# Kernel tuning notes

Measured on AMD Instinct MI355X. Metric: run time of the kernel, lower is better.

The kernel has to match this reference:

```python
import jax, jax.numpy as jnp
import numpy as np

# RReLU in eval mode == LeakyReLU with slope (lower+upper)/2, defaults 1/8, 1/3
RRELU_SLOPE = (1.0 / 8.0 + 1.0 / 3.0) / 2.0


def rrelu(x):
    return jnp.where(x >= 0, x, x * RRELU_SLOPE)


def _linear_params(key, fan_in, fan_out):
    kw, kb = jax.random.split(key)
    s = 1.0 / np.sqrt(fan_in)
    W = jax.random.uniform(kw, (fan_in, fan_out), minval=-s, maxval=s, dtype=jnp.float32)
    b = jax.random.uniform(kb, (fan_out,), minval=-s, maxval=s, dtype=jnp.float32)
    return W, b


def setup_inputs() -> dict:
    key = jax.random.key(0)
    ks = jax.random.split(key, 6)
    B, L, D_TS, D_SEQ, HID = 64, 2048, 8, 120, 64
    DIN = D_TS + D_SEQ
    ts = jax.random.normal(ks[0], (B, L, D_TS), dtype=jnp.float32)
    seq = jax.random.normal(ks[1], (B, L, D_SEQ), dtype=jnp.float32)
    lengths = jax.random.randint(ks[2], (B,), 1, L + 1, dtype=jnp.int32)
    Wk, bk = _linear_params(ks[3], DIN, HID)
    Wq, bq = _linear_params(ks[4], DIN, HID)
    Wv, bv = _linear_params(ks[5], DIN, HID)
    return {"ts": ts, "seq": seq, "lengths": lengths,
            "Wk": Wk, "bk": bk, "Wq": Wq, "bq": bq, "Wv": Wv, "bv": bv}


def reference(ts, seq, lengths, Wk, bk, Wq, bq, Wv, bv):
    # packed_cat([ts, seq]) -> concat along feature dim; padded positions masked later
    x = jnp.concatenate([ts, seq], axis=-1)              # [B, L, Din]
    k = rrelu(jnp.einsum('bld,dh->blh', x, Wk) + bk)     # [B, L, H]
    v = rrelu(jnp.einsum('bld,dh->blh', x, Wv) + bv)     # [B, L, H]
    q = rrelu(jnp.einsum('bld,dh->blh', x, Wq) + bq)     # [B, L, H]
    B, L, _ = x.shape
    # get_last_vectors_unpadded: last valid token of each sequence
    q_last = q[jnp.arange(B), lengths - 1]               # [B, H]
    scores = jnp.einsum('bh,blh->bl', q_last, k)         # [B, L]
    valid = jnp.arange(L)[None, :] < lengths[:, None]    # [B, L]
    scores = jnp.where(valid, scores, -jnp.inf)
    attn = jax.nn.softmax(scores, axis=-1)               # masked softmax over seq
    return jnp.einsum('bl,blh->bh', attn, v)             # [B, H]
```

## Files before the change

### kernel.cpp

```cpp
#include <hip/hip_runtime.h>
#include <hip/hip_bf16.h>

#define B_   64
#define L_   2048
#define DTS  8
#define DSEQ 120
#define DIN  128
#define H_   64
#define TILE 64
#define NT   (L_ / TILE)

typedef unsigned short u16;
typedef __bf16 bf16x8 __attribute__((ext_vector_type(8)));
typedef float  f32x4  __attribute__((ext_vector_type(4)));

__device__ __forceinline__ float rrelu_f(float x) {
    return x >= 0.f ? x : x * 0.22916666666666666f;
}

__device__ __forceinline__ u16 f2bf(float x) {
    unsigned u = __float_as_uint(x);
    return (u16)((u + 0x7FFFu + ((u >> 16) & 1u)) >> 16);
}
__device__ __forceinline__ float bf2f(u16 u) {
    return __uint_as_float(((unsigned)u) << 16);
}

__global__ void prep_kernel(const float* __restrict__ Wk, const float* __restrict__ Wv,
                            u16* __restrict__ pkh, u16* __restrict__ pkl,
                            u16* __restrict__ pvh, u16* __restrict__ pvl)
{
    const int f = blockIdx.x * 256 + threadIdx.x;
    const int idx = f & 8191;
    const bool isK = f < 8192;
    const float* W = isK ? Wk : Wv;
    u16* hi = isK ? pkh : pvh;
    u16* lo = isK ? pkl : pvl;
    const int j = idx & 7, lane = (idx >> 3) & 63, kk = (idx >> 9) & 3, ni = idx >> 11;
    const int kd = kk * 32 + (lane >> 4) * 8 + j;
    const int n  = ni * 16 + (lane & 15);
    const float v = W[kd * H_ + n];
    const u16 h = f2bf(v);
    hi[idx] = h;
    lo[idx] = f2bf(v - bf2f(h));
}

__global__ void qlast_kernel(const float* __restrict__ ts, const float* __restrict__ seq,
                             const int* __restrict__ lengths,
                             const float* __restrict__ Wq, const float* __restrict__ bq,
                             float* __restrict__ qlast)
{
    const int b = blockIdx.x, h = threadIdx.x;
    const int l = lengths[b] - 1;
    const float* tsr = ts  + ((size_t)b * L_ + l) * DTS;
    const float* sqr = seq + ((size_t)b * L_ + l) * DSEQ;
    float acc = bq[h];
    #pragma unroll
    for (int d = 0; d < DTS; ++d)  acc += tsr[d] * Wq[d * H_ + h];
    for (int d = 0; d < DSEQ; ++d) acc += sqr[d] * Wq[(DTS + d) * H_ + h];
    qlast[b * H_ + h] = rrelu_f(acc);
}

__global__ __launch_bounds__(256) void tile_kernel(
    const float* __restrict__ ts, const float* __restrict__ seq,
    const int* __restrict__ lengths,
    const u16* __restrict__ pkh, const u16* __restrict__ pkl,
    const u16* __restrict__ pvh, const u16* __restrict__ pvl,
    const float* __restrict__ bk, const float* __restrict__ bv,
    const float* __restrict__ qlast,
    float* __restrict__ pm, float* __restrict__ pd, float* __restrict__ pacc)
{
    const int b = blockIdx.y, t = blockIdx.x;
    const int tid = threadIdx.x;
    const int len = lengths[b];
    const int ls = t * TILE;
    const int pbase = b * NT + t;

    if (ls >= len) {
        if (tid < H_) pacc[(size_t)pbase * H_ + tid] = 0.f;
        if (tid == 0) { pm[pbase] = -INFINITY; pd[pbase] = 0.f; }
        return;
    }
    const int nv = min(TILE, len - ls);

    __shared__ __align__(16) u16 xh[TILE][136];
    __shared__ __align__(16) u16 xl[TILE][136];
    __shared__ float k_s[TILE][65];
    __shared__ float v_s[TILE][65];
    __shared__ float qls[H_];
    __shared__ float sc[TILE];
    __shared__ float red[4][H_];

    for (int c = tid; c < TILE * 32; c += 256) {
        const int row = c >> 5, ch = c & 31;
        const float* src = (ch < 2)
            ? ts  + ((size_t)b * L_ + ls + row) * DTS  + ch * 4
            : seq + ((size_t)b * L_ + ls + row) * DSEQ + (ch - 2) * 4;
        const float4 v = *(const float4*)src;
        const u16 h0 = f2bf(v.x), h1 = f2bf(v.y), h2 = f2bf(v.z), h3 = f2bf(v.w);
        const u16 g0 = f2bf(v.x - bf2f(h0)), g1 = f2bf(v.y - bf2f(h1));
        const u16 g2 = f2bf(v.z - bf2f(h2)), g3 = f2bf(v.w - bf2f(h3));
        unsigned* ph = (unsigned*)&xh[row][ch * 4];
        unsigned* pl = (unsigned*)&xl[row][ch * 4];
        ph[0] = (unsigned)h0 | ((unsigned)h1 << 16);
        ph[1] = (unsigned)h2 | ((unsigned)h3 << 16);
        pl[0] = (unsigned)g0 | ((unsigned)g1 << 16);
        pl[1] = (unsigned)g2 | ((unsigned)g3 << 16);
    }
    if (tid < H_) qls[tid] = qlast[b * H_ + tid];
    __syncthreads();

    const int wave = tid >> 6, lane = tid & 63;
    const int quad = lane >> 4, l16 = lane & 15;
    const int m0 = wave * 16;

    const u16* hrow = &xh[m0 + l16][0];
    const u16* lrow = &xl[m0 + l16][0];
    bf16x8 ah[4], al[4];
    #pragma unroll
    for (int kk = 0; kk < 4; ++kk) {
        ah[kk] = *(const bf16x8*)(hrow + kk * 32 + quad * 8);
        al[kk] = *(const bf16x8*)(lrow + kk * 32 + quad * 8);
    }

    #pragma unroll
    for (int ni = 0; ni < 4; ++ni) {
        const int n = ni * 16 + l16;
        f32x4 ak = {0.f, 0.f, 0.f, 0.f};
        f32x4 av = {0.f, 0.f, 0.f, 0.f};
        #pragma unroll
        for (int kk = 0; kk < 4; ++kk) {
            const size_t off = (size_t)(((ni * 4 + kk) * 64 + lane)) * 8;
            const bf16x8 bkh = *(const bf16x8*)(pkh + off);
            const bf16x8 bkl = *(const bf16x8*)(pkl + off);
            const bf16x8 bvh = *(const bf16x8*)(pvh + off);
            const bf16x8 bvl = *(const bf16x8*)(pvl + off);
            ak = __builtin_amdgcn_mfma_f32_16x16x32_bf16(ah[kk], bkh, ak, 0, 0, 0);
            ak = __builtin_amdgcn_mfma_f32_16x16x32_bf16(al[kk], bkh, ak, 0, 0, 0);
            ak = __builtin_amdgcn_mfma_f32_16x16x32_bf16(ah[kk], bkl, ak, 0, 0, 0);
            av = __builtin_amdgcn_mfma_f32_16x16x32_bf16(ah[kk], bvh, av, 0, 0, 0);
            av = __builtin_amdgcn_mfma_f32_16x16x32_bf16(al[kk], bvh, av, 0, 0, 0);
            av = __builtin_amdgcn_mfma_f32_16x16x32_bf16(ah[kk], bvl, av, 0, 0, 0);
        }
        const float bbk = bk[n], bbv = bv[n];
        #pragma unroll
        for (int r = 0; r < 4; ++r) {
            const int row = m0 + quad * 4 + r;
            k_s[row][n] = rrelu_f(ak[r] + bbk);
            v_s[row][n] = rrelu_f(av[r] + bbv);
        }
    }
    __syncthreads();

    if (wave == 0) {
        const int l = lane;
        float s = 0.f;
        #pragma unroll 8
        for (int h = 0; h < H_; ++h) s += qls[h] * k_s[l][h];
        if (l >= nv) s = -INFINITY;
        float m = s;
        #pragma unroll
        for (int off = 32; off; off >>= 1) m = fmaxf(m, __shfl_xor(m, off));
        const float p = __expf(s - m);
        float d = p;
        #pragma unroll
        for (int off = 32; off; off >>= 1) d += __shfl_xor(d, off);
        sc[l] = p;
        if (lane == 0) { pm[pbase] = m; pd[pbase] = d; }
    }
    __syncthreads();

    {
        const int h = lane;
        float acc = 0.f;
        #pragma unroll
        for (int i = 0; i < 16; ++i)
            acc += sc[wave * 16 + i] * v_s[wave * 16 + i][h];
        red[wave][h] = acc;
    }
    __syncthreads();
    if (tid < H_)
        pacc[(size_t)pbase * H_ + tid] = red[0][tid] + red[1][tid] + red[2][tid] + red[3][tid];
}

__global__ void combine_kernel(const float* __restrict__ pm, const float* __restrict__ pd,
                               const float* __restrict__ pacc, float* __restrict__ out)
{
    const int b = blockIdx.x, h = threadIdx.x;
    float m = -INFINITY;
    for (int t = 0; t < NT; ++t) m = fmaxf(m, pm[b * NT + t]);
    float den = 0.f, num = 0.f;
    for (int t = 0; t < NT; ++t) {
        const float w = __expf(pm[b * NT + t] - m);
        den += pd[b * NT + t] * w;
        num += pacc[(size_t)(b * NT + t) * H_ + h] * w;
    }
    out[b * H_ + h] = num / den;
}

extern "C" void kernel_launch(void* const* d_in, const int* in_sizes, int n_in,
                              void* d_out, int out_size, void* d_ws, size_t ws_size,
                              hipStream_t stream)
{
    const float* ts      = (const float*)d_in[0];
    const float* seq     = (const float*)d_in[1];
    const int*   lengths = (const int*)d_in[2];
    const float* Wk      = (const float*)d_in[3];
    const float* bk      = (const float*)d_in[4];
    const float* Wq      = (const float*)d_in[5];
    const float* bq      = (const float*)d_in[6];
    const float* Wv      = (const float*)d_in[7];
    const float* bv      = (const float*)d_in[8];

    float* ws    = (float*)d_ws;
    float* qlast = ws;
    float* pm    = ws + 4096;
    float* pd    = ws + 6144;
    float* pacc  = ws + 8192;
    u16*  packw  = (u16*)(ws + 139264);
    u16* pkh = packw;
    u16* pkl = packw + 8192;
    u16* pvh = packw + 16384;
    u16* pvl = packw + 24576;

    prep_kernel<<<dim3(64), dim3(256), 0, stream>>>(Wk, Wv, pkh, pkl, pvh, pvl);
    qlast_kernel<<<dim3(B_), dim3(H_), 0, stream>>>(ts, seq, lengths, Wq, bq, qlast);
    tile_kernel<<<dim3(NT, B_), dim3(256), 0, stream>>>(ts, seq, lengths,
                                                        pkh, pkl, pvh, pvl, bk, bv,
                                                        qlast, pm, pd, pacc);
    combine_kernel<<<dim3(B_), dim3(H_), 0, stream>>>(pm, pd, pacc, (float*)d_out);
}
```

Before: 145.3 us.

## Fuse setup kernels, DMA x to LDS, register-resident K/V, last-block combine

Merges the weight-packing and q_last kernels into one setup launch. The combine step is folded into the tile kernel through a per-batch atomic counter, so the last finishing block does the final reduction. Each block now handles two tiles and loads x with global_load_lds into swizzled fp32 LDS, splitting it into bf16 hi/lo in registers. Scores and the P·V product are computed from MFMA accumulators with shuffles instead of staging K and V through shared memory. This removes two launches and much LDS traffic, at the cost of atomics and fewer blocks in the grid.

Result: slower. 251.2 us (+72.8%).

```diff
diff --git a/kernel.cpp b/kernel.cpp
--- a/kernel.cpp
+++ b/kernel.cpp
@@ -5,19 +5,20 @@
 #define L_   2048
 #define DTS  8
 #define DSEQ 120
-#define DIN  128
 #define H_   64
 #define TILE 64
-#define NT   (L_ / TILE)
+#define NT   32
+#define TPB  2
+#define GX   (NT/TPB)
 
 typedef unsigned short u16;
 typedef __bf16 bf16x8 __attribute__((ext_vector_type(8)));
+typedef short  short8 __attribute__((ext_vector_type(8)));
 typedef float  f32x4  __attribute__((ext_vector_type(4)));
 
 __device__ __forceinline__ float rrelu_f(float x) {
     return x >= 0.f ? x : x * 0.22916666666666666f;
 }
-
 __device__ __forceinline__ u16 f2bf(float x) {
     unsigned u = __float_as_uint(x);
     return (u16)((u + 0x7FFFu + ((u >> 16) & 1u)) >> 16);
@@ -25,177 +26,229 @@
 __device__ __forceinline__ float bf2f(u16 u) {
     return __uint_as_float(((unsigned)u) << 16);
 }
-
-__global__ void prep_kernel(const float* __restrict__ Wk, const float* __restrict__ Wv,
-                            u16* __restrict__ pkh, u16* __restrict__ pkl,
-                            u16* __restrict__ pvh, u16* __restrict__ pvl)
+__device__ __forceinline__ void dma16(void* lds, const void* g) {
+    __builtin_amdgcn_global_load_lds(
+        (const __attribute__((address_space(1))) unsigned*)g,
+        (__attribute__((address_space(3))) unsigned*)lds, 16, 0, 0);
+}
+
+__global__ void setup_kernel(const float* __restrict__ ts, const float* __restrict__ seq,
+                             const int* __restrict__ lengths,
+                             const float* __restrict__ Wk, const float* __restrict__ Wv,
+                             const float* __restrict__ Wq, const float* __restrict__ bq,
+                             u16* __restrict__ pkh, u16* __restrict__ pkl,
+                             u16* __restrict__ pvh, u16* __restrict__ pvl,
+                             float* __restrict__ qlast, unsigned* __restrict__ cnt)
 {
-    const int f = blockIdx.x * 256 + threadIdx.x;
-    const int idx = f & 8191;
-    const bool isK = f < 8192;
-    const float* W = isK ? Wk : Wv;
-    u16* hi = isK ? pkh : pvh;
-    u16* lo = isK ? pkl : pvl;
-    const int j = idx & 7, lane = (idx >> 3) & 63, kk = (idx >> 9) & 3, ni = idx >> 11;
-    const int kd = kk * 32 + (lane >> 4) * 8 + j;
-    const int n  = ni * 16 + (lane & 15);
-    const float v = W[kd * H_ + n];
-    const u16 h = f2bf(v);
-    hi[idx] = h;
-    lo[idx] = f2bf(v - bf2f(h));
-}
-
-__global__ void qlast_kernel(const float* __restrict__ ts, const float* __restrict__ seq,
-                             const int* __restrict__ lengths,
-                             const float* __restrict__ Wq, const float* __restrict__ bq,
-                             float* __restrict__ qlast)
-{
-    const int b = blockIdx.x, h = threadIdx.x;
-    const int l = lengths[b] - 1;
-    const float* tsr = ts  + ((size_t)b * L_ + l) * DTS;
-    const float* sqr = seq + ((size_t)b * L_ + l) * DSEQ;
-    float acc = bq[h];
-    #pragma unroll
-    for (int d = 0; d < DTS; ++d)  acc += tsr[d] * Wq[d * H_ + h];
-    for (int d = 0; d < DSEQ; ++d) acc += sqr[d] * Wq[(DTS + d) * H_ + h];
-    qlast[b * H_ + h] = rrelu_f(acc);
-}
-
-__global__ __launch_bounds__(256) void tile_kernel(
+    const int blk = blockIdx.x, tid = threadIdx.x;
+    if (blk < 64) {
+        const int f = blk * 256 + tid;
+        const int idx = f & 8191;
+        const bool isK = f < 8192;
+        const float* W = isK ? Wk : Wv;
+        u16* hi = isK ? pkh : pvh;
+        u16* lo = isK ? pkl : pvl;
+        const int j = idx & 7, lane = (idx >> 3) & 63, kk = (idx >> 9) & 3, ni = idx >> 11;
+        const int kd = kk * 32 + (lane >> 4) * 8 + j;
+        const int n  = ni * 16 + (lane & 15);
+        const float v = W[kd * H_ + n];
+        const u16 h = f2bf(v);
+        hi[idx] = h;
+        lo[idx] = f2bf(v - bf2f(h));
+    } else if (blk < 80) {
+        const int b = (blk - 64) * 4 + (tid >> 6), h = tid & 63;
+        const int l = lengths[b] - 1;
+        const float* tsr = ts  + ((size_t)b * L_ + l) * DTS;
+        const float* sqr = seq + ((size_t)b * L_ + l) * DSEQ;
+        float acc = bq[h];
+        #pragma unroll
+        for (int d = 0; d < DTS; ++d)  acc += tsr[d] * Wq[d * H_ + h];
+        for (int d = 0; d < DSEQ; ++d) acc += sqr[d] * Wq[(DTS + d) * H_ + h];
+        qlast[b * H_ + h] = rrelu_f(acc);
+    } else {
+        if (tid < B_) cnt[tid] = 0u;
+    }
+}
+
+__global__ __launch_bounds__(256, 4) void tile_kernel(
     const float* __restrict__ ts, const float* __restrict__ seq,
     const int* __restrict__ lengths,
     const u16* __restrict__ pkh, const u16* __restrict__ pkl,
     const u16* __restrict__ pvh, const u16* __restrict__ pvl,
     const float* __restrict__ bk, const float* __restrict__ bv,
     const float* __restrict__ qlast,
-    float* __restrict__ pm, float* __restrict__ pd, float* __restrict__ pacc)
+    float* __restrict__ pm, float* __restrict__ pd, float* __restrict__ pacc,
+    unsigned* __restrict__ cnt, float* __restrict__ out)
 {
-    const int b = blockIdx.y, t = blockIdx.x;
-    const int tid = threadIdx.x;
+    const int b = blockIdx.y, g = blockIdx.x, tid = threadIdx.x;
     const int len = lengths[b];
-    const int ls = t * TILE;
-    const int pbase = b * NT + t;
-
-    if (ls >= len) {
-        if (tid < H_) pacc[(size_t)pbase * H_ + tid] = 0.f;
-        if (tid == 0) { pm[pbase] = -INFINITY; pd[pbase] = 0.f; }
-        return;
-    }
-    const int nv = min(TILE, len - ls);
-
-    __shared__ __align__(16) u16 xh[TILE][136];
-    __shared__ __align__(16) u16 xl[TILE][136];
-    __shared__ float k_s[TILE][65];
-    __shared__ float v_s[TILE][65];
-    __shared__ float qls[H_];
+    const int wave = tid >> 6, lane = tid & 63, quad = lane >> 4, l16 = lane & 15;
+    const int m0 = wave * 16;
+
+    __shared__ __align__(16) float xs[TILE * 128];
     __shared__ float sc[TILE];
     __shared__ float red[4][H_];
-
-    for (int c = tid; c < TILE * 32; c += 256) {
-        const int row = c >> 5, ch = c & 31;
-        const float* src = (ch < 2)
-            ? ts  + ((size_t)b * L_ + ls + row) * DTS  + ch * 4
-            : seq + ((size_t)b * L_ + ls + row) * DSEQ + (ch - 2) * 4;
-        const float4 v = *(const float4*)src;
-        const u16 h0 = f2bf(v.x), h1 = f2bf(v.y), h2 = f2bf(v.z), h3 = f2bf(v.w);
-        const u16 g0 = f2bf(v.x - bf2f(h0)), g1 = f2bf(v.y - bf2f(h1));
-        const u16 g2 = f2bf(v.z - bf2f(h2)), g3 = f2bf(v.w - bf2f(h3));
-        unsigned* ph = (unsigned*)&xh[row][ch * 4];
-        unsigned* pl = (unsigned*)&xl[row][ch * 4];
-        ph[0] = (unsigned)h0 | ((unsigned)h1 << 16);
-        ph[1] = (unsigned)h2 | ((unsigned)h3 << 16);
-        pl[0] = (unsigned)g0 | ((unsigned)g1 << 16);
-        pl[1] = (unsigned)g2 | ((unsigned)g3 << 16);
-    }
-    if (tid < H_) qls[tid] = qlast[b * H_ + tid];
-    __syncthreads();
-
-    const int wave = tid >> 6, lane = tid & 63;
-    const int quad = lane >> 4, l16 = lane & 15;
-    const int m0 = wave * 16;
-
-    const u16* hrow = &xh[m0 + l16][0];
-    const u16* lrow = &xl[m0 + l16][0];
-    bf16x8 ah[4], al[4];
-    #pragma unroll
-    for (int kk = 0; kk < 4; ++kk) {
-        ah[kk] = *(const bf16x8*)(hrow + kk * 32 + quad * 8);
-        al[kk] = *(const bf16x8*)(lrow + kk * 32 + quad * 8);
-    }
-
+    __shared__ float wd[4];
+    __shared__ int winflag;
+
+    float q4[4], bbk[4], bbv[4];
     #pragma unroll
     for (int ni = 0; ni < 4; ++ni) {
-        const int n = ni * 16 + l16;
-        f32x4 ak = {0.f, 0.f, 0.f, 0.f};
-        f32x4 av = {0.f, 0.f, 0.f, 0.f};
-        #pragma unroll
-        for (int kk = 0; kk < 4; ++kk) {
-            const size_t off = (size_t)(((ni * 4 + kk) * 64 + lane)) * 8;
-            const bf16x8 bkh = *(const bf16x8*)(pkh + off);
-            const bf16x8 bkl = *(const bf16x8*)(pkl + off);
-            const bf16x8 bvh = *(const bf16x8*)(pvh + off);
-            const bf16x8 bvl = *(const bf16x8*)(pvl + off);
-            ak = __builtin_amdgcn_mfma_f32_16x16x32_bf16(ah[kk], bkh, ak, 0, 0, 0);
-            ak = __builtin_amdgcn_mfma_f32_16x16x32_bf16(al[kk], bkh, ak, 0, 0, 0);
-            ak = __builtin_amdgcn_mfma_f32_16x16x32_bf16(ah[kk], bkl, ak, 0, 0, 0);
-            av = __builtin_amdgcn_mfma_f32_16x16x32_bf16(ah[kk], bvh, av, 0, 0, 0);
-            av = __builtin_amdgcn_mfma_f32_16x16x32_bf16(al[kk], bvh, av, 0, 0, 0);
-            av = __builtin_amdgcn_mfma_f32_16x16x32_bf16(ah[kk], bvl, av, 0, 0, 0);
-        }
-        const float bbk = bk[n], bbv = bv[n];
+        q4[ni]  = qlast[b * H_ + ni * 16 + l16];
+        bbk[ni] = bk[ni * 16 + l16];
+        bbv[ni] = bv[ni * 16 + l16];
+    }
+
+    for (int it = 0; it < TPB; ++it) {
+        const int t = g * TPB + it, ls = t * TILE, pb = b * NT + t;
+        if (ls >= len) {
+            if (tid < H_)
+                __hip_atomic_store(&pacc[(size_t)pb * H_ + tid], 0.f,
+                                   __ATOMIC_RELAXED, __HIP_MEMORY_SCOPE_AGENT);
+            if (tid == 0) {
+                __hip_atomic_store(&pm[pb], -INFINITY, __ATOMIC_RELAXED, __HIP_MEMORY_SCOPE_AGENT);
+                __hip_atomic_store(&pd[pb], 0.f, __ATOMIC_RELAXED, __HIP_MEMORY_SCOPE_AGENT);
+            }
+            continue;
+        }
+        const int nv = min(TILE, len - ls);
+
+        __syncthreads();
+        #pragma unroll
+        for (int i = 0; i < 8; ++i) {
+            const int CI = wave * 512 + i * 64 + lane;
+            const int row = CI >> 5, cp = CI & 31;
+            const int c = cp ^ (row & 7);
+            void* dst = (void*)((char*)xs + (size_t)(wave * 512 + i * 64) * 16);
+            if (c < 2) dma16(dst, ts  + ((size_t)(b * L_ + ls + row)) * DTS  + c * 4);
+            else       dma16(dst, seq + ((size_t)(b * L_ + ls + row)) * DSEQ + (c - 2) * 4);
+        }
+        __syncthreads();
+
+        bf16x8 ah[4], al[4];
+        {
+            const int row = m0 + l16;
+            const float* rb = xs + row * 128;
+            #pragma unroll
+            for (int kk = 0; kk < 4; ++kk) {
+                const int c0 = kk * 8 + quad * 2;
+                const f32x4 u = *(const f32x4*)(rb + (c0 ^ (l16 & 7)) * 4);
+                const f32x4 w = *(const f32x4*)(rb + ((c0 + 1) ^ (l16 & 7)) * 4);
+                short8 h8, l8;
+                #pragma unroll
+                for (int j = 0; j < 4; ++j) {
+                    const u16 hu = f2bf(u[j]); h8[j] = (short)hu; l8[j] = (short)f2bf(u[j] - bf2f(hu));
+                    const u16 hw = f2bf(w[j]); h8[4+j] = (short)hw; l8[4+j] = (short)f2bf(w[j] - bf2f(hw));
+                }
+                ah[kk] = __builtin_bit_cast(bf16x8, h8);
+                al[kk] = __builtin_bit_cast(bf16x8, l8);
+            }
+        }
+
+        float ps[4] = {0.f, 0.f, 0.f, 0.f};
+        float vv[4][4];
+        #pragma unroll
+        for (int ni = 0; ni < 4; ++ni) {
+            f32x4 ak = {0.f, 0.f, 0.f, 0.f};
+            f32x4 av = {0.f, 0.f, 0.f, 0.f};
+            #pragma unroll
+            for (int kk = 0; kk < 4; ++kk) {
+                const size_t off = (size_t)((ni * 4 + kk) * 64 + lane) * 8;
+                const bf16x8 bkh = *(const bf16x8*)(pkh + off);
+                const bf16x8 bkl = *(const bf16x8*)(pkl + off);
+                const bf16x8 bvh = *(const bf16x8*)(pvh + off);
+                const bf16x8 bvl = *(const bf16x8*)(pvl + off);
+                ak = __builtin_amdgcn_mfma_f32_16x16x32_bf16(ah[kk], bkh, ak, 0, 0, 0);
+                ak = __builtin_amdgcn_mfma_f32_16x16x32_bf16(al[kk], bkh, ak, 0, 0, 0);
+                ak = __builtin_amdgcn_mfma_f32_16x16x32_bf16(ah[kk], bkl, ak, 0, 0, 0);
+                av = __builtin_amdgcn_mfma_f32_16x16x32_bf16(ah[kk], bvh, av, 0, 0, 0);
+                av = __builtin_amdgcn_mfma_f32_16x16x32_bf16(al[kk], bvh, av, 0, 0, 0);
+                av = __builtin_amdgcn_mfma_f32_16x16x32_bf16(ah[kk], bvl, av, 0, 0, 0);
+            }
+            #pragma unroll
+            for (int r = 0; r < 4; ++r) {
+                const float kv = rrelu_f(ak[r] + bbk[ni]);
+                vv[ni][r] = rrelu_f(av[r] + bbv[ni]);
+                ps[r] += q4[ni] * kv;
+            }
+        }
+        #pragma unroll
+        for (int mk = 1; mk < 16; mk <<= 1) {
+            #pragma unroll
+            for (int r = 0; r < 4; ++r) ps[r] += __shfl_xor(ps[r], mk);
+        }
         #pragma unroll
         for (int r = 0; r < 4; ++r) {
             const int row = m0 + quad * 4 + r;
-            k_s[row][n] = rrelu_f(ak[r] + bbk);
-            v_s[row][n] = rrelu_f(av[r] + bbv);
-        }
-    }
+            if (row >= nv) ps[r] = -INFINITY;
+            if (l16 == 0) sc[row] = ps[r];
+        }
+        __syncthreads();
+
+        float mv = sc[lane];
+        #pragma unroll
+        for (int mk = 1; mk < 64; mk <<= 1) mv = fmaxf(mv, __shfl_xor(mv, mk));
+
+        float p[4], dsum = 0.f, pv[4];
+        #pragma unroll
+        for (int r = 0; r < 4; ++r) { p[r] = __expf(ps[r] - mv); dsum += p[r]; }
+        #pragma unroll
+        for (int ni = 0; ni < 4; ++ni) {
+            float a = 0.f;
+            #pragma unroll
+            for (int r = 0; r < 4; ++r) a += p[r] * vv[ni][r];
+            pv[ni] = a;
+        }
+        #pragma unroll
+        for (int mk = 16; mk < 64; mk <<= 1) {
+            #pragma unroll
+            for (int ni = 0; ni < 4; ++ni) pv[ni] += __shfl_xor(pv[ni], mk);
+            dsum += __shfl_xor(dsum, mk);
+        }
+        if (quad == 0) {
+            #pragma unroll
+            for (int ni = 0; ni < 4; ++ni) red[wave][ni * 16 + l16] = pv[ni];
+        }
+        if (lane == 0) wd[wave] = dsum;
+        __syncthreads();
+
+        if (tid < H_) {
+            const float a = red[0][tid] + red[1][tid] + red[2][tid] + red[3][tid];
+            __hip_atomic_store(&pacc[(size_t)pb * H_ + tid], a,
+                               __ATOMIC_RELAXED, __HIP_MEMORY_SCOPE_AGENT);
+        }
+        if (tid == 0) {
+            __hip_atomic_store(&pm[pb], mv, __ATOMIC_RELAXED, __HIP_MEMORY_SCOPE_AGENT);
+            __hip_atomic_store(&pd[pb], wd[0] + wd[1] + wd[2] + wd[3],
+                               __ATOMIC_RELAXED, __HIP_MEMORY_SCOPE_AGENT);
+        }
+    }
+
     __syncthreads();
-
-    if (wave == 0) {
-        const int l = lane;
-        float s = 0.f;
-        #pragma unroll 8
-        for (int h = 0; h < H_; ++h) s += qls[h] * k_s[l][h];
-        if (l >= nv) s = -INFINITY;
-        float m = s;
-        #pragma unroll
-        for (int off = 32; off; off >>= 1) m = fmaxf(m, __shfl_xor(m, off));
-        const float p = __expf(s - m);
-        float d = p;
-        #pragma unroll
-        for (int off = 32; off; off >>= 1) d += __shfl_xor(d, off);
-        sc[l] = p;
-        if (lane == 0) { pm[pbase] = m; pd[pbase] = d; }
+    if (tid == 0) {
+        const unsigned old = __hip_atomic_fetch_add(&cnt[b], 1u,
+                                __ATOMIC_ACQ_REL, __HIP_MEMORY_SCOPE_AGENT);
+        winflag = (old == GX - 1) ? 1 : 0;
     }
     __syncthreads();
-
-    {
-        const int h = lane;
-        float acc = 0.f;
-        #pragma unroll
-        for (int i = 0; i < 16; ++i)
-            acc += sc[wave * 16 + i] * v_s[wave * 16 + i][h];
-        red[wave][h] = acc;
-    }
-    __syncthreads();
-    if (tid < H_)
-        pacc[(size_t)pbase * H_ + tid] = red[0][tid] + red[1][tid] + red[2][tid] + red[3][tid];
-}
-
-__global__ void combine_kernel(const float* __restrict__ pm, const float* __restrict__ pd,
-                               const float* __restrict__ pacc, float* __restrict__ out)
-{
-    const int b = blockIdx.x, h = threadIdx.x;
-    float m = -INFINITY;
-    for (int t = 0; t < NT; ++t) m = fmaxf(m, pm[b * NT + t]);
-    float den = 0.f, num = 0.f;
-    for (int t = 0; t < NT; ++t) {
-        const float w = __expf(pm[b * NT + t] - m);
-        den += pd[b * NT + t] * w;
-        num += pacc[(size_t)(b * NT + t) * H_ + h] * w;
-    }
-    out[b * H_ + h] = num / den;
+    if (winflag && tid < H_) {
+        const int h = tid;
+        float m = -INFINITY;
+        for (int t2 = 0; t2 < NT; ++t2)
+            m = fmaxf(m, __hip_atomic_load(&pm[b * NT + t2],
+                          __ATOMIC_RELAXED, __HIP_MEMORY_SCOPE_AGENT));
+        float den = 0.f, num = 0.f;
+        for (int t2 = 0; t2 < NT; ++t2) {
+            const float mm = __hip_atomic_load(&pm[b * NT + t2],
+                               __ATOMIC_RELAXED, __HIP_MEMORY_SCOPE_AGENT);
+            const float w = __expf(mm - m);
+            den += __hip_atomic_load(&pd[b * NT + t2],
+                     __ATOMIC_RELAXED, __HIP_MEMORY_SCOPE_AGENT) * w;
+            num += __hip_atomic_load(&pacc[(size_t)(b * NT + t2) * H_ + h],
+                     __ATOMIC_RELAXED, __HIP_MEMORY_SCOPE_AGENT) * w;
+        }
+        out[b * H_ + h] = num / den;
+    }
 }
 
 extern "C" void kernel_launch(void* const* d_in, const int* in_sizes, int n_in,
@@ -217,16 +270,16 @@
     float* pm    = ws + 4096;
     float* pd    = ws + 6144;
     float* pacc  = ws + 8192;
-    u16*  packw  = (u16*)(ws + 139264);
+    u16*   packw = (u16*)(ws + 139264);
     u16* pkh = packw;
     u16* pkl = packw + 8192;
     u16* pvh = packw + 16384;
     u16* pvl = packw + 24576;
-
-    prep_kernel<<<dim3(64), dim3(256), 0, stream>>>(Wk, Wv, pkh, pkl, pvh, pvl);
-    qlast_kernel<<<dim3(B_), dim3(H_), 0, stream>>>(ts, seq, lengths, Wq, bq, qlast);
-    tile_kernel<<<dim3(NT, B_), dim3(256), 0, stream>>>(ts, seq, lengths,
+    unsigned* cnt = (unsigned*)(ws + 155648);
+
+    setup_kernel<<<dim3(81), dim3(256), 0, stream>>>(ts, seq, lengths, Wk, Wv, Wq, bq,
+                                                     pkh, pkl, pvh, pvl, qlast, cnt);
+    tile_kernel<<<dim3(GX, B_), dim3(256), 0, stream>>>(ts, seq, lengths,
                                                         pkh, pkl, pvh, pvl, bk, bv,
-                                                        qlast, pm, pd, pacc);
-    combine_kernel<<<dim3(B_), dim3(H_), 0, stream>>>(pm, pd, pacc, (float*)d_out);
-}
+                                                        qlast, pm, pd, pacc, cnt, (float*)d_out);
+}
```
